# Kernel tuning notes

Measured on AMD Instinct MI355X. Metric: run time of the kernel, lower is better.

The kernel has to match this reference:

```python
import jax, jax.numpy as jnp
import numpy as np

B, T, C, H = 64, 512, 384, 64

def setup_inputs() -> dict:
    key = jax.random.key(0)
    ks = jax.random.split(key, 7)
    s = 0.02
    return {
        "x": jax.random.normal(ks[0], (B, T, C), dtype=jnp.float32),
        "Wq": jax.random.normal(ks[1], (C, H), dtype=jnp.float32) * s,
        "bq": jax.random.normal(ks[2], (H,), dtype=jnp.float32) * s,
        "Wk": jax.random.normal(ks[3], (C, H), dtype=jnp.float32) * s,
        "bk": jax.random.normal(ks[4], (H,), dtype=jnp.float32) * s,
        "Wv": jax.random.normal(ks[5], (C, H), dtype=jnp.float32) * s,
        "bv": jax.random.normal(ks[6], (H,), dtype=jnp.float32) * s,
    }

def reference(x, Wq, bq, Wk, bk, Wv, bv):
    # single-head causal self-attention (dropout in eval mode -> identity)
    q = x @ Wq + bq                      # [B,T,H]
    k = x @ Wk + bk                      # [B,T,H]
    v = x @ Wv + bv                      # [B,T,H]
    scale = jnp.asarray(k.shape[-1], x.dtype) ** -0.5
    scores = jnp.einsum('bth,bsh->bts', q, k) * scale   # [B,T,T]
    t = scores.shape[-1]
    causal = jnp.tril(jnp.ones((t, t), dtype=bool))
    scores = jnp.where(causal, scores, jnp.asarray(-jnp.inf, scores.dtype))
    attn = jax.nn.softmax(scores, axis=-1)               # [B,T,T]
    out = jnp.einsum('bts,bsh->bth', attn, v)            # [B,T,H]
    return out
```

## Files before the change

### kernel.cpp

```cpp
#include <hip/hip_runtime.h>
#include <math.h>

#define BB 64
#define TT 512
#define CC 384
#define HH 64
#define MM (BB*TT)

#define QSCALE 0.18033688011112042f

typedef __attribute__((ext_vector_type(8))) short short8;
typedef __attribute__((ext_vector_type(4))) float f32x4;

__device__ __forceinline__ unsigned short f2bf(float f) {
    union { float f; unsigned int u; } x; x.f = f;
    unsigned int r = x.u + 0x7fff + ((x.u >> 16) & 1);
    return (unsigned short)(r >> 16);
}

__global__ __launch_bounds__(256) void prep_w(
    const float* __restrict__ Wq, const float* __restrict__ Wk,
    const float* __restrict__ Wv, unsigned short* __restrict__ Wt)
{
    __shared__ float t[64][65];
    const int which = blockIdx.x / 6;
    const int kt    = blockIdx.x % 6;
    const float* W = (which == 0) ? Wq : (which == 1) ? Wk : Wv;
    const float sc = (which == 0) ? QSCALE : 1.f;
    const int tid = threadIdx.x;
    #pragma unroll
    for (int i = 0; i < 16; i++) {
        int idx = tid + i * 256;
        int kl = idx >> 6, n = idx & 63;
        t[kl][n] = W[(size_t)(kt * 64 + kl) * HH + n];
    }
    __syncthreads();
    #pragma unroll
    for (int i = 0; i < 16; i++) {
        int idx = tid + i * 256;
        int nl = idx >> 6, kl = idx & 63;
        Wt[(size_t)(which * 64 + nl) * CC + kt * 64 + kl] = f2bf(t[kl][nl] * sc);
    }
}

__global__ __launch_bounds__(256) void qkv_proj_mfma(
    const float* __restrict__ x, const unsigned short* __restrict__ Wt,
    const float* __restrict__ bq, const float* __restrict__ bk,
    const float* __restrict__ bv,
    unsigned short* __restrict__ qb, unsigned short* __restrict__ kb,
    unsigned short* __restrict__ vt)
{
    __shared__ unsigned short xs[64][CC + 8];
    const int tid  = threadIdx.x;
    const int w    = tid >> 6;
    const int lane = tid & 63;
    const int l15  = lane & 15;
    const int lg   = lane >> 4;
    const int rows0 = blockIdx.x * 64;

    #pragma unroll
    for (int kc = 0; kc < 6; kc++) {
        #pragma unroll
        for (int i = 0; i < 4; i++) {
            int idx = tid + i * 256;
            int row = idx >> 4, j4 = idx & 15;
            const float4 xv = *reinterpret_cast<const float4*>(
                &x[(size_t)(rows0 + row) * CC + kc * 64 + j4 * 4]);
            ushort4 pk;
            pk.x = f2bf(xv.x); pk.y = f2bf(xv.y);
            pk.z = f2bf(xv.z); pk.w = f2bf(xv.w);
            *reinterpret_cast<ushort4*>(&xs[row][kc * 64 + j4 * 4]) = pk;
        }
    }
    __syncthreads();

    f32x4 acc[4][3];
    #pragma unroll
    for (int mi = 0; mi < 4; mi++)
        #pragma unroll
        for (int f = 0; f < 3; f++) acc[mi][f] = (f32x4){0.f, 0.f, 0.f, 0.f};

    #pragma unroll 4
    for (int ks = 0; ks < 12; ks++) {
        short8 afrag[4];
        #pragma unroll
        for (int mi = 0; mi < 4; mi++)
            afrag[mi] = *reinterpret_cast<const short8*>(
                &xs[mi * 16 + l15][ks * 32 + lg * 8]);
        #pragma unroll
        for (int f = 0; f < 3; f++) {
            const int n = w * 48 + f * 16 + l15;
            const short8 bfrag = *reinterpret_cast<const short8*>(
                &Wt[(size_t)n * CC + ks * 32 + lg * 8]);
            #pragma unroll
            for (int mi = 0; mi < 4; mi++)
                acc[mi][f] = __builtin_amdgcn_mfma_f32_16x16x32_bf16(
                    afrag[mi], bfrag, acc[mi][f], 0, 0, 0);
        }
    }

    const int batch = rows0 >> 9;
    const int t0    = rows0 & 511;

    __syncthreads();
    unsigned short (*L)[72] = reinterpret_cast<unsigned short (*)[72]>(&xs[0][0]);

    #pragma unroll
    for (int f = 0; f < 3; f++) {
        const int c = w * 48 + f * 16 + l15;
        if (c < 64) {
            const float bb = bq[c] * QSCALE;
            #pragma unroll
            for (int mi = 0; mi < 4; mi++)
                #pragma unroll
                for (int rr = 0; rr < 4; rr++)
                    L[mi * 16 + lg * 4 + rr][c] = f2bf(acc[mi][f][rr] + bb);
        } else if (c < 128) {
            const int ci = c - 64;
            const float bb = bk[ci];
            #pragma unroll
            for (int mi = 0; mi < 4; mi++)
                #pragma unroll
                for (int rr = 0; rr < 4; rr++)
                    L[64 + mi * 16 + lg * 4 + rr][ci] = f2bf(acc[mi][f][rr] + bb);
        } else {
            const int ci = c - 128;
            const float bb = bv[ci];
            #pragma unroll
            for (int mi = 0; mi < 4; mi++) {
                ushort4 pk;
                pk.x = f2bf(acc[mi][f][0] + bb);
                pk.y = f2bf(acc[mi][f][1] + bb);
                pk.z = f2bf(acc[mi][f][2] + bb);
                pk.w = f2bf(acc[mi][f][3] + bb);
                *reinterpret_cast<ushort4*>(
                    &vt[((size_t)batch * HH + ci) * TT + t0 + mi * 16 + lg * 4]) = pk;
            }
        }
    }
    __syncthreads();

    #pragma unroll
    for (int i = 0; i < 4; i++) {
        int idx = tid + i * 256;
        int r = idx >> 3, c8 = idx & 7;
        const short8 val = *reinterpret_cast<const short8*>(&L[r][c8 * 8]);
        if (r < 64)
            *reinterpret_cast<short8*>(&qb[(size_t)(rows0 + r) * HH + c8 * 8]) = val;
        else
            *reinterpret_cast<short8*>(&kb[(size_t)(rows0 + r - 64) * HH + c8 * 8]) = val;
    }
}

__global__ __launch_bounds__(64, 2) void attn_mfma(
    const unsigned short* __restrict__ q, const unsigned short* __restrict__ k,
    const unsigned short* __restrict__ vt, float* __restrict__ out)
{
    __shared__ unsigned short P[16][72];
    const int lane = threadIdx.x;
    const int l15  = lane & 15;
    const int lg   = lane >> 4;
    const int qs   = blockIdx.x >> 6;
    const int b    = blockIdx.x & 63;
    const int qr0  = b * TT + qs * 16;

    const unsigned short* __restrict__ kbase = k  + (size_t)b * TT * HH;
    const unsigned short* __restrict__ vbase = vt + (size_t)b * HH * TT;

    short8 aq[2];
    #pragma unroll
    for (int ks = 0; ks < 2; ks++)
        aq[ks] = *reinterpret_cast<const short8*>(
            &q[(size_t)(qr0 + l15) * HH + ks * 32 + lg * 8]);

    f32x4 accO[4];
    #pragma unroll
    for (int nf = 0; nf < 4; nf++) accO[nf] = (f32x4){0.f, 0.f, 0.f, 0.f};
    float lsum[4] = {0.f, 0.f, 0.f, 0.f};

    const int ntiles = (qs >> 2) + 1;

#define LOADK(dst, j)                                                          \
    _Pragma("unroll")                                                          \
    for (int ks = 0; ks < 2; ks++)                                             \
        _Pragma("unroll")                                                      \
        for (int nf = 0; nf < 4; nf++)                                         \
            dst[ks][nf] = *reinterpret_cast<const short8*>(                    \
                &kbase[(size_t)((j) * 64 + nf * 16 + l15) * HH + ks * 32 + lg * 8]);

    short8 kf[2][4];
    LOADK(kf, 0);

    for (int j = 0; j < ntiles; ++j) {
        f32x4 s[4];
        #pragma unroll
        for (int nf = 0; nf < 4; nf++) s[nf] = (f32x4){0.f, 0.f, 0.f, 0.f};
        #pragma unroll
        for (int ks = 0; ks < 2; ks++)
            #pragma unroll
            for (int nf = 0; nf < 4; nf++)
                s[nf] = __builtin_amdgcn_mfma_f32_16x16x32_bf16(
                    aq[ks], kf[ks][nf], s[nf], 0, 0, 0);

        short8 vf[2][4];
        #pragma unroll
        for (int ks = 0; ks < 2; ks++)
            #pragma unroll
            for (int nf = 0; nf < 4; nf++)
                vf[ks][nf] = *reinterpret_cast<const short8*>(
                    &vbase[(size_t)(nf * 16 + l15) * TT + j * 64 + ks * 32 + lg * 8]);

        const int jn = (j + 1 < ntiles) ? j + 1 : j;
        short8 kfn[2][4];
        LOADK(kfn, jn);

        float p[4][4];
        if (j == ntiles - 1) {
            #pragma unroll
            for (int nf = 0; nf < 4; nf++)
                #pragma unroll
                for (int rg = 0; rg < 4; rg++)
                    p[nf][rg] = (j * 64 + nf * 16 + l15 > qs * 16 + lg * 4 + rg)
                                ? 0.f : exp2f(s[nf][rg]);
        } else {
            #pragma unroll
            for (int nf = 0; nf < 4; nf++)
                #pragma unroll
                for (int rg = 0; rg < 4; rg++)
                    p[nf][rg] = exp2f(s[nf][rg]);
        }
        #pragma unroll
        for (int rg = 0; rg < 4; rg++)
            lsum[rg] += (p[0][rg] + p[1][rg]) + (p[2][rg] + p[3][rg]);

        #pragma unroll
        for (int nf = 0; nf < 4; nf++)
            #pragma unroll
            for (int rg = 0; rg < 4; rg++)
                P[lg * 4 + rg][nf * 16 + l15] = f2bf(p[nf][rg]);

        #pragma unroll
        for (int ks = 0; ks < 2; ks++) {
            const short8 pa = *reinterpret_cast<const short8*>(
                &P[l15][ks * 32 + lg * 8]);
            #pragma unroll
            for (int nf = 0; nf < 4; nf++)
                accO[nf] = __builtin_amdgcn_mfma_f32_16x16x32_bf16(
                    pa, vf[ks][nf], accO[nf], 0, 0, 0);
        }

        #pragma unroll
        for (int ks = 0; ks < 2; ks++)
            #pragma unroll
            for (int nf = 0; nf < 4; nf++)
                kf[ks][nf] = kfn[ks][nf];
    }
#undef LOADK

    float inv[4];
    #pragma unroll
    for (int rg = 0; rg < 4; rg++) {
        float l = lsum[rg];
        l += __shfl_xor(l, 1);
        l += __shfl_xor(l, 2);
        l += __shfl_xor(l, 4);
        l += __shfl_xor(l, 8);
        inv[rg] = 1.f / l;
    }
    #pragma unroll
    for (int nf = 0; nf < 4; nf++)
        #pragma unroll
        for (int rg = 0; rg < 4; rg++)
            out[(size_t)(qr0 + lg * 4 + rg) * HH + nf * 16 + l15] =
                accO[nf][rg] * inv[rg];
}

extern "C" void kernel_launch(void* const* d_in, const int* in_sizes, int n_in,
                              void* d_out, int out_size, void* d_ws, size_t ws_size,
                              hipStream_t stream) {
    const float* x  = (const float*)d_in[0];
    const float* Wq = (const float*)d_in[1];
    const float* bq = (const float*)d_in[2];
    const float* Wk = (const float*)d_in[3];
    const float* bk = (const float*)d_in[4];
    const float* Wv = (const float*)d_in[5];
    const float* bv = (const float*)d_in[6];
    float* out = (float*)d_out;

    unsigned short* qb = (unsigned short*)d_ws;
    unsigned short* kb = qb + (size_t)MM * HH;
    unsigned short* vt = kb + (size_t)MM * HH;
    unsigned short* Wt = vt + (size_t)MM * HH;

    prep_w<<<dim3(18), dim3(256), 0, stream>>>(Wq, Wk, Wv, Wt);
    qkv_proj_mfma<<<dim3(MM / 64), dim3(256), 0, stream>>>(
        x, Wt, bq, bk, bv, qb, kb, vt);
    attn_mfma<<<dim3(2048), dim3(64), 0, stream>>>(qb, kb, vt, out);
}
```

Measured before the change: 50.71 us.

## Software-pipeline attention loop with double-buffered P and halve projection tile rows

The attention loop is restructured so the QK^T MFMAs for tile j are issued alongside the PV accumulation of tile j-1. The P buffer in LDS is double-buffered and the V loads are moved one iteration ahead. This is meant to overlap exp/softmax work, LDS round trips and global loads with matrix-core work. Separately, the QKV projection now uses 32-row tiles instead of 64, doubling the grid to get more blocks per CU at the cost of reloading W fragments more often.

```diff
diff --git a/kernel.cpp b/kernel.cpp
--- a/kernel.cpp
+++ b/kernel.cpp
@@ -50,18 +50,18 @@
     unsigned short* __restrict__ qb, unsigned short* __restrict__ kb,
     unsigned short* __restrict__ vt)
 {
-    __shared__ unsigned short xs[64][CC + 8];
+    __shared__ unsigned short xs[32][CC + 8];
     const int tid  = threadIdx.x;
     const int w    = tid >> 6;
     const int lane = tid & 63;
     const int l15  = lane & 15;
     const int lg   = lane >> 4;
-    const int rows0 = blockIdx.x * 64;
+    const int rows0 = blockIdx.x * 32;
 
     #pragma unroll
     for (int kc = 0; kc < 6; kc++) {
         #pragma unroll
-        for (int i = 0; i < 4; i++) {
+        for (int i = 0; i < 2; i++) {
             int idx = tid + i * 256;
             int row = idx >> 4, j4 = idx & 15;
             const float4 xv = *reinterpret_cast<const float4*>(
@@ -74,17 +74,17 @@
     }
     __syncthreads();
 
-    f32x4 acc[4][3];
-    #pragma unroll
-    for (int mi = 0; mi < 4; mi++)
+    f32x4 acc[2][3];
+    #pragma unroll
+    for (int mi = 0; mi < 2; mi++)
         #pragma unroll
         for (int f = 0; f < 3; f++) acc[mi][f] = (f32x4){0.f, 0.f, 0.f, 0.f};
 
     #pragma unroll 4
     for (int ks = 0; ks < 12; ks++) {
-        short8 afrag[4];
-        #pragma unroll
-        for (int mi = 0; mi < 4; mi++)
+        short8 afrag[2];
+        #pragma unroll
+        for (int mi = 0; mi < 2; mi++)
             afrag[mi] = *reinterpret_cast<const short8*>(
                 &xs[mi * 16 + l15][ks * 32 + lg * 8]);
         #pragma unroll
@@ -93,7 +93,7 @@
             const short8 bfrag = *reinterpret_cast<const short8*>(
                 &Wt[(size_t)n * CC + ks * 32 + lg * 8]);
             #pragma unroll
-            for (int mi = 0; mi < 4; mi++)
+            for (int mi = 0; mi < 2; mi++)
                 acc[mi][f] = __builtin_amdgcn_mfma_f32_16x16x32_bf16(
                     afrag[mi], bfrag, acc[mi][f], 0, 0, 0);
         }
@@ -111,7 +111,7 @@
         if (c < 64) {
             const float bb = bq[c] * QSCALE;
             #pragma unroll
-            for (int mi = 0; mi < 4; mi++)
+            for (int mi = 0; mi < 2; mi++)
                 #pragma unroll
                 for (int rr = 0; rr < 4; rr++)
                     L[mi * 16 + lg * 4 + rr][c] = f2bf(acc[mi][f][rr] + bb);
@@ -119,15 +119,15 @@
             const int ci = c - 64;
             const float bb = bk[ci];
             #pragma unroll
-            for (int mi = 0; mi < 4; mi++)
+            for (int mi = 0; mi < 2; mi++)
                 #pragma unroll
                 for (int rr = 0; rr < 4; rr++)
-                    L[64 + mi * 16 + lg * 4 + rr][ci] = f2bf(acc[mi][f][rr] + bb);
+                    L[32 + mi * 16 + lg * 4 + rr][ci] = f2bf(acc[mi][f][rr] + bb);
         } else {
             const int ci = c - 128;
             const float bb = bv[ci];
             #pragma unroll
-            for (int mi = 0; mi < 4; mi++) {
+            for (int mi = 0; mi < 2; mi++) {
                 ushort4 pk;
                 pk.x = f2bf(acc[mi][f][0] + bb);
                 pk.y = f2bf(acc[mi][f][1] + bb);
@@ -141,14 +141,14 @@
     __syncthreads();
 
     #pragma unroll
-    for (int i = 0; i < 4; i++) {
+    for (int i = 0; i < 2; i++) {
         int idx = tid + i * 256;
         int r = idx >> 3, c8 = idx & 7;
         const short8 val = *reinterpret_cast<const short8*>(&L[r][c8 * 8]);
-        if (r < 64)
+        if (r < 32)
             *reinterpret_cast<short8*>(&qb[(size_t)(rows0 + r) * HH + c8 * 8]) = val;
         else
-            *reinterpret_cast<short8*>(&kb[(size_t)(rows0 + r - 64) * HH + c8 * 8]) = val;
+            *reinterpret_cast<short8*>(&kb[(size_t)(rows0 + r - 32) * HH + c8 * 8]) = val;
     }
 }
 
@@ -156,7 +156,7 @@
     const unsigned short* __restrict__ q, const unsigned short* __restrict__ k,
     const unsigned short* __restrict__ vt, float* __restrict__ out)
 {
-    __shared__ unsigned short P[16][72];
+    __shared__ unsigned short P[2][16][72];
     const int lane = threadIdx.x;
     const int l15  = lane & 15;
     const int lg   = lane >> 4;
@@ -178,7 +178,7 @@
     for (int nf = 0; nf < 4; nf++) accO[nf] = (f32x4){0.f, 0.f, 0.f, 0.f};
     float lsum[4] = {0.f, 0.f, 0.f, 0.f};
 
-    const int ntiles = (qs >> 2) + 1;
+    const int n = (qs >> 2) + 1;
 
 #define LOADK(dst, j)                                                          \
     _Pragma("unroll")                                                          \
@@ -187,75 +187,86 @@
         for (int nf = 0; nf < 4; nf++)                                         \
             dst[ks][nf] = *reinterpret_cast<const short8*>(                    \
                 &kbase[(size_t)((j) * 64 + nf * 16 + l15) * HH + ks * 32 + lg * 8]);
-
-    short8 kf[2][4];
+#define LOADV(dst, j)                                                          \
+    _Pragma("unroll")                                                          \
+    for (int ks = 0; ks < 2; ks++)                                             \
+        _Pragma("unroll")                                                      \
+        for (int nf = 0; nf < 4; nf++)                                         \
+            dst[ks][nf] = *reinterpret_cast<const short8*>(                    \
+                &vbase[(size_t)(nf * 16 + l15) * TT + (j) * 64 + ks * 32 + lg * 8]);
+
+#define QKT(s, kf)                                                             \
+    _Pragma("unroll")                                                          \
+    for (int nf = 0; nf < 4; nf++) s[nf] = (f32x4){0.f, 0.f, 0.f, 0.f};        \
+    _Pragma("unroll")                                                          \
+    for (int ks = 0; ks < 2; ks++)                                             \
+        _Pragma("unroll")                                                      \
+        for (int nf = 0; nf < 4; nf++)                                         \
+            s[nf] = __builtin_amdgcn_mfma_f32_16x16x32_bf16(aq[ks], kf[ks][nf], s[nf], 0, 0, 0);
+
+#define EXPP(s, j, pb)                                                         \
+    {                                                                          \
+        float p_[4][4];                                                        \
+        if ((j) == n - 1) {                                                    \
+            _Pragma("unroll")                                                  \
+            for (int nf = 0; nf < 4; nf++)                                     \
+                _Pragma("unroll")                                              \
+                for (int rg = 0; rg < 4; rg++)                                 \
+                    p_[nf][rg] = ((j) * 64 + nf * 16 + l15 > qs * 16 + lg * 4 + rg) \
+                                 ? 0.f : exp2f(s[nf][rg]);                     \
+        } else {                                                               \
+            _Pragma("unroll")                                                  \
+            for (int nf = 0; nf < 4; nf++)                                     \
+                _Pragma("unroll")                                              \
+                for (int rg = 0; rg < 4; rg++)                                 \
+                    p_[nf][rg] = exp2f(s[nf][rg]);                             \
+        }                                                                      \
+        _Pragma("unroll")                                                      \
+        for (int rg = 0; rg < 4; rg++)                                         \
+            lsum[rg] += (p_[0][rg] + p_[1][rg]) + (p_[2][rg] + p_[3][rg]);     \
+        _Pragma("unroll")                                                      \
+        for (int nf = 0; nf < 4; nf++)                                         \
+            _Pragma("unroll")                                                  \
+            for (int rg = 0; rg < 4; rg++)                                     \
+                P[pb][lg * 4 + rg][nf * 16 + l15] = f2bf(p_[nf][rg]);          \
+    }
+
+#define PVACC(pb, vf)                                                          \
+    _Pragma("unroll")                                                          \
+    for (int ks = 0; ks < 2; ks++) {                                           \
+        const short8 pa = *reinterpret_cast<const short8*>(                    \
+            &P[pb][l15][ks * 32 + lg * 8]);                                    \
+        _Pragma("unroll")                                                      \
+        for (int nf = 0; nf < 4; nf++)                                         \
+            accO[nf] = __builtin_amdgcn_mfma_f32_16x16x32_bf16(                \
+                pa, vf[ks][nf], accO[nf], 0, 0, 0);                            \
+    }
+
+    short8 kf[2][4], vf[2][4];
+
     LOADK(kf, 0);
-
-    for (int j = 0; j < ntiles; ++j) {
-        f32x4 s[4];
-        #pragma unroll
-        for (int nf = 0; nf < 4; nf++) s[nf] = (f32x4){0.f, 0.f, 0.f, 0.f};
-        #pragma unroll
-        for (int ks = 0; ks < 2; ks++)
-            #pragma unroll
-            for (int nf = 0; nf < 4; nf++)
-                s[nf] = __builtin_amdgcn_mfma_f32_16x16x32_bf16(
-                    aq[ks], kf[ks][nf], s[nf], 0, 0, 0);
-
-        short8 vf[2][4];
-        #pragma unroll
-        for (int ks = 0; ks < 2; ks++)
-            #pragma unroll
-            for (int nf = 0; nf < 4; nf++)
-                vf[ks][nf] = *reinterpret_cast<const short8*>(
-                    &vbase[(size_t)(nf * 16 + l15) * TT + j * 64 + ks * 32 + lg * 8]);
-
-        const int jn = (j + 1 < ntiles) ? j + 1 : j;
-        short8 kfn[2][4];
-        LOADK(kfn, jn);
-
-        float p[4][4];
-        if (j == ntiles - 1) {
-            #pragma unroll
-            for (int nf = 0; nf < 4; nf++)
-                #pragma unroll
-                for (int rg = 0; rg < 4; rg++)
-                    p[nf][rg] = (j * 64 + nf * 16 + l15 > qs * 16 + lg * 4 + rg)
-                                ? 0.f : exp2f(s[nf][rg]);
-        } else {
-            #pragma unroll
-            for (int nf = 0; nf < 4; nf++)
-                #pragma unroll
-                for (int rg = 0; rg < 4; rg++)
-                    p[nf][rg] = exp2f(s[nf][rg]);
-        }
-        #pragma unroll
-        for (int rg = 0; rg < 4; rg++)
-            lsum[rg] += (p[0][rg] + p[1][rg]) + (p[2][rg] + p[3][rg]);
-
-        #pragma unroll
-        for (int nf = 0; nf < 4; nf++)
-            #pragma unroll
-            for (int rg = 0; rg < 4; rg++)
-                P[lg * 4 + rg][nf * 16 + l15] = f2bf(p[nf][rg]);
-
-        #pragma unroll
-        for (int ks = 0; ks < 2; ks++) {
-            const short8 pa = *reinterpret_cast<const short8*>(
-                &P[l15][ks * 32 + lg * 8]);
-            #pragma unroll
-            for (int nf = 0; nf < 4; nf++)
-                accO[nf] = __builtin_amdgcn_mfma_f32_16x16x32_bf16(
-                    pa, vf[ks][nf], accO[nf], 0, 0, 0);
-        }
-
-        #pragma unroll
-        for (int ks = 0; ks < 2; ks++)
-            #pragma unroll
-            for (int nf = 0; nf < 4; nf++)
-                kf[ks][nf] = kfn[ks][nf];
-    }
+    f32x4 s[4];
+    QKT(s, kf);
+    LOADV(vf, 0);
+    if (n > 1) LOADK(kf, 1);
+    EXPP(s, 0, 0);
+
+    for (int j = 1; j < n; ++j) {
+        QKT(s, kf);
+        PVACC((j - 1) & 1, vf);
+        LOADV(vf, j);
+        const int jn = (j + 1 < n) ? j + 1 : n - 1;
+        LOADK(kf, jn);
+        EXPP(s, j, j & 1);
+    }
+
+    PVACC((n - 1) & 1, vf);
+
 #undef LOADK
+#undef LOADV
+#undef QKT
+#undef EXPP
+#undef PVACC
 
     float inv[4];
     #pragma unroll
@@ -293,7 +304,7 @@
     unsigned short* Wt = vt + (size_t)MM * HH;
 
     prep_w<<<dim3(18), dim3(256), 0, stream>>>(Wq, Wk, Wv, Wt);
-    qkv_proj_mfma<<<dim3(MM / 64), dim3(256), 0, stream>>>(
+    qkv_proj_mfma<<<dim3(MM / 32), dim3(256), 0, stream>>>(
         x, Wt, bq, bk, bv, qb, kb, vt);
     attn_mfma<<<dim3(2048), dim3(64), 0, stream>>>(qb, kb, vt, out);
 }
```

Result: slower. 57.23 us (+12.9%).

## Split attention KV tiles across four waves per block with LDS combine

Applied to the files above, without the earlier changes.

Each attention block now runs four waves that take interleaved 64-key tiles of the causal range, each keeping partial output accumulators and row sums, then reducing them through shared memory before normalising and writing. This is meant to cut the serial per-block latency of the long causal rows and raise the number of waves in flight. In exchange it drops the register double-buffered K prefetch, adds a block barrier and an LDS reduction, and leaves waves idle on early query tiles that have fewer key tiles than waves.

```diff
diff --git a/kernel.cpp b/kernel.cpp
--- a/kernel.cpp
+++ b/kernel.cpp
@@ -152,17 +152,22 @@
     }
 }
 
-__global__ __launch_bounds__(64, 2) void attn_mfma(
+__global__ __launch_bounds__(256, 3) void attn_mfma(
     const unsigned short* __restrict__ q, const unsigned short* __restrict__ k,
     const unsigned short* __restrict__ vt, float* __restrict__ out)
 {
-    __shared__ unsigned short P[16][72];
-    const int lane = threadIdx.x;
+    __shared__ float Cmb[4][16][68];
+    __shared__ float Ls[4][16];
+    __shared__ unsigned short P[4][16][72];
+    const int tid  = threadIdx.x;
+    const int w    = tid >> 6;
+    const int lane = tid & 63;
     const int l15  = lane & 15;
     const int lg   = lane >> 4;
     const int qs   = blockIdx.x >> 6;
     const int b    = blockIdx.x & 63;
     const int qr0  = b * TT + qs * 16;
+    const int n    = (qs >> 2) + 1;
 
     const unsigned short* __restrict__ kbase = k  + (size_t)b * TT * HH;
     const unsigned short* __restrict__ vbase = vt + (size_t)b * HH * TT;
@@ -178,20 +183,14 @@
     for (int nf = 0; nf < 4; nf++) accO[nf] = (f32x4){0.f, 0.f, 0.f, 0.f};
     float lsum[4] = {0.f, 0.f, 0.f, 0.f};
 
-    const int ntiles = (qs >> 2) + 1;
-
-#define LOADK(dst, j)                                                          \
-    _Pragma("unroll")                                                          \
-    for (int ks = 0; ks < 2; ks++)                                             \
-        _Pragma("unroll")                                                      \
-        for (int nf = 0; nf < 4; nf++)                                         \
-            dst[ks][nf] = *reinterpret_cast<const short8*>(                    \
-                &kbase[(size_t)((j) * 64 + nf * 16 + l15) * HH + ks * 32 + lg * 8]);
-
-    short8 kf[2][4];
-    LOADK(kf, 0);
-
-    for (int j = 0; j < ntiles; ++j) {
+    for (int j = w; j < n; j += 4) {
+        short8 kf[2][4];
+        #pragma unroll
+        for (int ks = 0; ks < 2; ks++)
+            #pragma unroll
+            for (int nf = 0; nf < 4; nf++)
+                kf[ks][nf] = *reinterpret_cast<const short8*>(
+                    &kbase[(size_t)(j * 64 + nf * 16 + l15) * HH + ks * 32 + lg * 8]);
         f32x4 s[4];
         #pragma unroll
         for (int nf = 0; nf < 4; nf++) s[nf] = (f32x4){0.f, 0.f, 0.f, 0.f};
@@ -210,12 +209,8 @@
                 vf[ks][nf] = *reinterpret_cast<const short8*>(
                     &vbase[(size_t)(nf * 16 + l15) * TT + j * 64 + ks * 32 + lg * 8]);
 
-        const int jn = (j + 1 < ntiles) ? j + 1 : j;
-        short8 kfn[2][4];
-        LOADK(kfn, jn);
-
         float p[4][4];
-        if (j == ntiles - 1) {
+        if (j == n - 1) {
             #pragma unroll
             for (int nf = 0; nf < 4; nf++)
                 #pragma unroll
@@ -237,27 +232,19 @@
         for (int nf = 0; nf < 4; nf++)
             #pragma unroll
             for (int rg = 0; rg < 4; rg++)
-                P[lg * 4 + rg][nf * 16 + l15] = f2bf(p[nf][rg]);
+                P[w][lg * 4 + rg][nf * 16 + l15] = f2bf(p[nf][rg]);
 
         #pragma unroll
         for (int ks = 0; ks < 2; ks++) {
             const short8 pa = *reinterpret_cast<const short8*>(
-                &P[l15][ks * 32 + lg * 8]);
+                &P[w][l15][ks * 32 + lg * 8]);
             #pragma unroll
             for (int nf = 0; nf < 4; nf++)
                 accO[nf] = __builtin_amdgcn_mfma_f32_16x16x32_bf16(
                     pa, vf[ks][nf], accO[nf], 0, 0, 0);
         }
-
-        #pragma unroll
-        for (int ks = 0; ks < 2; ks++)
-            #pragma unroll
-            for (int nf = 0; nf < 4; nf++)
-                kf[ks][nf] = kfn[ks][nf];
-    }
-#undef LOADK
-
-    float inv[4];
+    }
+
     #pragma unroll
     for (int rg = 0; rg < 4; rg++) {
         float l = lsum[rg];
@@ -265,14 +252,23 @@
         l += __shfl_xor(l, 2);
         l += __shfl_xor(l, 4);
         l += __shfl_xor(l, 8);
-        inv[rg] = 1.f / l;
+        if (l15 == 0) Ls[w][lg * 4 + rg] = l;
     }
     #pragma unroll
     for (int nf = 0; nf < 4; nf++)
         #pragma unroll
         for (int rg = 0; rg < 4; rg++)
-            out[(size_t)(qr0 + lg * 4 + rg) * HH + nf * 16 + l15] =
-                accO[nf][rg] * inv[rg];
+            Cmb[w][lg * 4 + rg][nf * 16 + l15] = accO[nf][rg];
+    __syncthreads();
+
+    #pragma unroll
+    for (int rg = 0; rg < 4; rg++) {
+        const int row = lg * 4 + rg;
+        const float ltot = Ls[0][row] + Ls[1][row] + Ls[2][row] + Ls[3][row];
+        const float sum = Cmb[0][row][w * 16 + l15] + Cmb[1][row][w * 16 + l15]
+                        + Cmb[2][row][w * 16 + l15] + Cmb[3][row][w * 16 + l15];
+        out[(size_t)(qr0 + row) * HH + w * 16 + l15] = sum / ltot;
+    }
 }
 
 extern "C" void kernel_launch(void* const* d_in, const int* in_sizes, int n_in,
@@ -295,5 +291,5 @@
     prep_w<<<dim3(18), dim3(256), 0, stream>>>(Wq, Wk, Wv, Wt);
     qkv_proj_mfma<<<dim3(MM / 64), dim3(256), 0, stream>>>(
         x, Wt, bq, bk, bv, qb, kb, vt);
-    attn_mfma<<<dim3(2048), dim3(64), 0, stream>>>(qb, kb, vt, out);
-}
+    attn_mfma<<<dim3(2048), dim3(256), 0, stream>>>(qb, kb, vt, out);
+}
```

Result: slower. 51.77 us (+2.1%).
